# Optimization experiments

Measured on AMD Instinct MI355X. Metric: run time of the kernel, lower is better.

The kernel has to match this reference:

```python
import jax, jax.numpy as jnp
import numpy as np

N_NODES = 100000
N_EDGES = 6400000
D = 12

def setup_inputs() -> dict:
    key = jax.random.key(0)
    k1, k2, k3, k4 = jax.random.split(key, 4)
    x = jax.random.normal(k1, (N_NODES, D), dtype=jnp.float32)
    W_l = jax.random.normal(k2, (D, D), dtype=jnp.float32) / np.sqrt(D)
    W_r = jax.random.normal(k3, (D, D), dtype=jnp.float32) / np.sqrt(D)
    b = jnp.zeros((D,), dtype=jnp.float32)
    edge_index = jax.random.randint(k4, (2, N_EDGES), 0, N_NODES, dtype=jnp.int64)
    return {"x": x, "W_l": W_l, "W_r": W_r, "b": b, "edge_index": edge_index}

def reference(x, W_l, W_r, b, edge_index):
    # PyG SAGEConv (mean aggregation): out = lin_l(mean_{j in N(i)} x_j) + lin_r(x_i)
    src = edge_index[0]
    dst = edge_index[1]
    n = x.shape[0]
    msgs = x[src]                                      # [E, D] gather
    agg = jax.ops.segment_sum(msgs, dst, num_segments=n)          # [N, D]
    cnt = jax.ops.segment_sum(jnp.ones_like(dst, dtype=x.dtype), dst, num_segments=n)
    mean = agg / jnp.maximum(cnt, 1.0)[:, None]        # [N, D]
    out = mean @ W_l.T + x @ W_r.T + b                 # lin_l carries the bias in PyG
    return out
```

## Files before the change

### kernel.cpp

```cpp
#include <hip/hip_runtime.h>

#define N_NODES 100000
#define N_EDGES 6400000
#define D 12

#define SLOG 7
#define SSZ  128
#define NB   ((N_NODES + SSZ - 1) / SSZ)
#define SBLK 256
#define STHR 512
#define SEPB (N_EDGES / SBLK)
#define RSTR 13

#define CAP  1792
#define EPT  (CAP / 256)

__device__ __forceinline__ unsigned int f2bf(float f) {
    unsigned int u = __float_as_uint(f);
    return (u + 0x7fffu + ((u >> 16) & 1u)) >> 16;
}
__device__ __forceinline__ unsigned int pk2(float lo, float hi) {
    return (f2bf(hi) << 16) | f2bf(lo);
}
__device__ __forceinline__ float bflo(unsigned int u) { return __uint_as_float(u << 16); }
__device__ __forceinline__ float bfhi(unsigned int u) { return __uint_as_float(u & 0xffff0000u); }

__global__ __launch_bounds__(256) void prep_kernel(
    const float* __restrict__ x, unsigned int* __restrict__ xb)
{
    int i = blockIdx.x * 256 + threadIdx.x;
    if (i >= N_NODES) return;
    const float4* xr = (const float4*)(x) + (size_t)i * 3;
    float4 a = xr[0], b = xr[1], c = xr[2];
    unsigned int* o = xb + (size_t)i * 8;
    ((uint4*)o)[0] = make_uint4(pk2(a.x, a.y), pk2(a.z, a.w), pk2(b.x, b.y), pk2(b.z, b.w));
    ((uint2*)(o + 4))[0] = make_uint2(pk2(c.x, c.y), pk2(c.z, c.w));
}

__global__ __launch_bounds__(512) void part_kernel(
    const int* __restrict__ ei, int* __restrict__ cnt, int* __restrict__ rowpre,
    unsigned int* __restrict__ sorted)
{
    __shared__ int h[NB];
    __shared__ int cur[NB];
    __shared__ int sb2[512];
    int t = threadIdx.x;
    int b = blockIdx.x;
    for (int i = t; i < NB; i += STHR) h[i] = 0;
    __syncthreads();

    const int* dei = ei + N_EDGES;
    int start = b * SEPB;
    int end = start + SEPB;

    int e = start + t;
    while (e + 3 * STHR < end) {
        int d0 = dei[e], d1 = dei[e + STHR], d2 = dei[e + 2 * STHR], d3 = dei[e + 3 * STHR];
        atomicAdd(&h[d0 >> SLOG], 1);
        atomicAdd(&h[d1 >> SLOG], 1);
        atomicAdd(&h[d2 >> SLOG], 1);
        atomicAdd(&h[d3 >> SLOG], 1);
        e += 4 * STHR;
    }
    while (e < end) { atomicAdd(&h[dei[e] >> SLOG], 1); e += STHR; }
    __syncthreads();

    int* crow = cnt + (size_t)b * NB;
    for (int i = t; i < NB; i += STHR) crow[i] = h[i];

    int pairv = 0;
    if (t < (NB + 1) / 2) {
        pairv = h[2 * t] + ((2 * t + 1 < NB) ? h[2 * t + 1] : 0);
    }
    sb2[t] = pairv;
    __syncthreads();
    for (int o = 1; o < 512; o <<= 1) {
        int v = (t >= o) ? sb2[t - o] : 0;
        __syncthreads();
        sb2[t] += v;
        __syncthreads();
    }
    if (t < (NB + 1) / 2) {
        int excl = sb2[t] - pairv;
        cur[2 * t] = excl;
        if (2 * t + 1 < NB) cur[2 * t + 1] = excl + h[2 * t];
    }
    __syncthreads();

    int* rrow = rowpre + (size_t)b * NB;
    for (int i = t; i < NB; i += STHR) rrow[i] = cur[i];
    __syncthreads();

    unsigned int* dst = sorted + (size_t)b * SEPB;
    e = start + t;
    while (e + 3 * STHR < end) {
        int s0 = ei[e], s1 = ei[e + STHR], s2 = ei[e + 2 * STHR], s3 = ei[e + 3 * STHR];
        int d0 = dei[e], d1 = dei[e + STHR], d2 = dei[e + 2 * STHR], d3 = dei[e + 3 * STHR];
        int p0 = atomicAdd(&cur[d0 >> SLOG], 1);
        int p1 = atomicAdd(&cur[d1 >> SLOG], 1);
        int p2 = atomicAdd(&cur[d2 >> SLOG], 1);
        int p3 = atomicAdd(&cur[d3 >> SLOG], 1);
        dst[p0] = ((unsigned)s0 << SLOG) | (unsigned)(d0 & (SSZ - 1));
        dst[p1] = ((unsigned)s1 << SLOG) | (unsigned)(d1 & (SSZ - 1));
        dst[p2] = ((unsigned)s2 << SLOG) | (unsigned)(d2 & (SSZ - 1));
        dst[p3] = ((unsigned)s3 << SLOG) | (unsigned)(d3 & (SSZ - 1));
        e += 4 * STHR;
    }
    while (e < end) {
        int s = ei[e], d = dei[e];
        int pos = atomicAdd(&cur[d >> SLOG], 1);
        dst[pos] = ((unsigned)s << SLOG) | (unsigned)(d & (SSZ - 1));
        e += STHR;
    }
}

__global__ __launch_bounds__(256) void agg_reg_kernel(
    const unsigned int* __restrict__ sorted, const int* __restrict__ cntm,
    const int* __restrict__ rowpre, const unsigned int* __restrict__ xb,
    const float* __restrict__ x, const float* __restrict__ Wl,
    const float* __restrict__ Wr, const float* __restrict__ bias,
    float* __restrict__ out)
{
    __shared__ float sWl[D * D], sWr[D * D], sb[D];
    __shared__ int cnt[SSZ];
    __shared__ int sbuf[SSZ];
    __shared__ int segbase[SSZ + 1];
    __shared__ int cursor[SSZ];
    __shared__ int cnt_tot[SSZ];
    __shared__ int seglen[SBLK];
    __shared__ int segoff[SBLK];
    __shared__ int segpre[SBLK + 1];
    __shared__ unsigned vals[CAP * 6];

    int t = threadIdx.x;
    int k = blockIdx.x;

    if (t < D * D) { sWl[t] = Wl[t]; sWr[t] = Wr[t]; }
    if (t < D) sb[t] = bias[t];
    if (t < SSZ) cnt_tot[t] = 0;

    if (t < SBLK) {
        seglen[t] = cntm[(size_t)t * NB + k];
        segoff[t] = t * SEPB + rowpre[(size_t)t * NB + k];
    }
    __syncthreads();
    int sl = (t < SBLK) ? seglen[t] : 0;
    if (t < SBLK) sbuf[0] = 0;
    {
        if (t < SBLK) segpre[t + 1] = sl;
        if (t == 0) segpre[0] = 0;
        __syncthreads();
        for (int o = 1; o < SBLK; o <<= 1) {
            int v = 0;
            if (t < SBLK && (int)t + 1 > o) v = segpre[t + 1 - o];
            __syncthreads();
            if (t < SBLK) segpre[t + 1] += v;
            __syncthreads();
        }
    }
    int T = segpre[SBLK];

    float acc[D];
#pragma unroll
    for (int d = 0; d < D; ++d) acc[d] = 0.f;

    int loc = t >> 1;
    int sub = t & 1;

    for (int c0 = 0; c0 < T; c0 += CAP) {
        int n = min(CAP, T - c0);
        if (t < SSZ) cnt[t] = 0;
        __syncthreads();

        unsigned pe[EPT];
        int ne = 0;
        for (int j = t; j < n; j += 256) {
            int v = c0 + j;
            int lo = 0, hi = SBLK;
            while (hi - lo > 1) {
                int mid = (lo + hi) >> 1;
                if (segpre[mid] <= v) lo = mid; else hi = mid;
            }
            int gi = segoff[lo] + (v - segpre[lo]);
            pe[ne++] = sorted[gi];
        }
#pragma unroll
        for (int q = 0; q < EPT; ++q)
            if (q < ne) atomicAdd(&cnt[pe[q] & (SSZ - 1)], 1);
        __syncthreads();

        if (t < SSZ) sbuf[t] = cnt[t];
        __syncthreads();
        for (int o = 1; o < SSZ; o <<= 1) {
            int v = (t < SSZ && t >= o) ? sbuf[t - o] : 0;
            __syncthreads();
            if (t < SSZ) sbuf[t] += v;
            __syncthreads();
        }
        if (t < SSZ) {
            segbase[t + 1] = sbuf[t];
            if (t == 0) segbase[0] = 0;
        }
        __syncthreads();
        if (t < SSZ) { cursor[t] = segbase[t]; cnt_tot[t] += cnt[t]; }
        __syncthreads();

#pragma unroll
        for (int q = 0; q < EPT; ++q) {
            if (q < ne) {
                unsigned p = pe[q];
                int slot = atomicAdd(&cursor[p & (SSZ - 1)], 1);
                const unsigned* r = xb + (size_t)(p >> SLOG) * 8;
                uint2 q0 = ((const uint2*)r)[0];
                uint2 q1 = ((const uint2*)r)[1];
                uint2 q2 = ((const uint2*)r)[2];
                unsigned* vv = &vals[slot * 6];
                ((uint2*)vv)[0] = q0;
                ((uint2*)vv)[1] = q1;
                ((uint2*)vv)[2] = q2;
            }
        }
        __syncthreads();

        int s0 = segbase[loc], s1 = segbase[loc + 1];
        for (int j = s0 + sub; j < s1; j += 2) {
            const unsigned* vv = &vals[j * 6];
            uint2 q0 = ((const uint2*)vv)[0];
            uint2 q1 = ((const uint2*)vv)[1];
            uint2 q2 = ((const uint2*)vv)[2];
            acc[0]  += bflo(q0.x); acc[1]  += bfhi(q0.x);
            acc[2]  += bflo(q0.y); acc[3]  += bfhi(q0.y);
            acc[4]  += bflo(q1.x); acc[5]  += bfhi(q1.x);
            acc[6]  += bflo(q1.y); acc[7]  += bfhi(q1.y);
            acc[8]  += bflo(q2.x); acc[9]  += bfhi(q2.x);
            acc[10] += bflo(q2.y); acc[11] += bfhi(q2.y);
        }
        __syncthreads();
    }

    float* red = (float*)vals;
#pragma unroll
    for (int d = 0; d < D; ++d) red[sub * 1664 + loc * 13 + d] = acc[d];
    __syncthreads();

    if (t < SSZ) {
        int node = k * SSZ + t;
        if (node < N_NODES) {
            float m[D];
#pragma unroll
            for (int d = 0; d < D; ++d)
                m[d] = red[t * 13 + d] + red[1664 + t * 13 + d];
            float inv = 1.f / fmaxf((float)cnt_tot[t], 1.f);
#pragma unroll
            for (int d = 0; d < D; ++d) m[d] *= inv;

            float xi[D];
            const float4* xr = (const float4*)(x) + (size_t)node * 3;
            float4 x0 = xr[0], x1 = xr[1], x2 = xr[2];
            xi[0] = x0.x; xi[1] = x0.y; xi[2]  = x0.z; xi[3]  = x0.w;
            xi[4] = x1.x; xi[5] = x1.y; xi[6]  = x1.z; xi[7]  = x1.w;
            xi[8] = x2.x; xi[9] = x2.y; xi[10] = x2.z; xi[11] = x2.w;

            float o[D];
#pragma unroll
            for (int oo = 0; oo < D; ++oo) {
                float a = sb[oo];
#pragma unroll
                for (int d = 0; d < D; ++d) {
                    a += m[d] * sWl[oo * D + d];
                    a += xi[d] * sWr[oo * D + d];
                }
                o[oo] = a;
            }
            float4* orow = (float4*)(out) + (size_t)node * 3;
            orow[0] = make_float4(o[0], o[1], o[2], o[3]);
            orow[1] = make_float4(o[4], o[5], o[6], o[7]);
            orow[2] = make_float4(o[8], o[9], o[10], o[11]);
        }
    }
}


__global__ __launch_bounds__(256) void scatter_kernel(
    const int* __restrict__ ei, const float* __restrict__ x,
    float* __restrict__ agg, float* __restrict__ cnt)
{
    int e = blockIdx.x * blockDim.x + threadIdx.x;
    if (e >= N_EDGES) return;
    int src = ei[e];
    int dst = ei[N_EDGES + e];
    const float4* xr = (const float4*)(x + (size_t)src * D);
    float4 a = xr[0], b4 = xr[1], c = xr[2];
    float* dr = agg + (size_t)dst * D;
    atomicAdd(dr + 0,  a.x);  atomicAdd(dr + 1,  a.y);
    atomicAdd(dr + 2,  a.z);  atomicAdd(dr + 3,  a.w);
    atomicAdd(dr + 4,  b4.x); atomicAdd(dr + 5,  b4.y);
    atomicAdd(dr + 6,  b4.z); atomicAdd(dr + 7,  b4.w);
    atomicAdd(dr + 8,  c.x);  atomicAdd(dr + 9,  c.y);
    atomicAdd(dr + 10, c.z);  atomicAdd(dr + 11, c.w);
    atomicAdd(cnt + dst, 1.0f);
}

__global__ __launch_bounds__(256) void finalize_kernel(
    const float* __restrict__ x, const float* __restrict__ Wl,
    const float* __restrict__ Wr, const float* __restrict__ bias,
    const float* __restrict__ agg, const float* __restrict__ cnt,
    float* __restrict__ out)
{
    __shared__ float sWl[D * D], sWr[D * D], sb[D];
    int t = threadIdx.x;
    if (t < D * D) { sWl[t] = Wl[t]; sWr[t] = Wr[t]; }
    if (t < D) sb[t] = bias[t];
    __syncthreads();
    int i = blockIdx.x * blockDim.x + t;
    if (i >= N_NODES) return;
    float inv = 1.0f / fmaxf(cnt[i], 1.0f);
    float m[D], xi[D];
    const float4* ar = (const float4*)(agg + (size_t)i * D);
    const float4* xr = (const float4*)(x + (size_t)i * D);
    float4 a0 = ar[0], a1 = ar[1], a2 = ar[2];
    float4 x0 = xr[0], x1 = xr[1], x2 = xr[2];
    m[0] = a0.x * inv; m[1] = a0.y * inv; m[2]  = a0.z * inv; m[3]  = a0.w * inv;
    m[4] = a1.x * inv; m[5] = a1.y * inv; m[6]  = a1.z * inv; m[7]  = a1.w * inv;
    m[8] = a2.x * inv; m[9] = a2.y * inv; m[10] = a2.z * inv; m[11] = a2.w * inv;
    xi[0] = x0.x; xi[1] = x0.y; xi[2]  = x0.z; xi[3]  = x0.w;
    xi[4] = x1.x; xi[5] = x1.y; xi[6]  = x1.z; xi[7]  = x1.w;
    xi[8] = x2.x; xi[9] = x2.y; xi[10] = x2.z; xi[11] = x2.w;
    float o[D];
#pragma unroll
    for (int oo = 0; oo < D; ++oo) {
        float acc = sb[oo];
#pragma unroll
        for (int d = 0; d < D; ++d) {
            acc += m[d] * sWl[oo * D + d];
            acc += xi[d] * sWr[oo * D + d];
        }
        o[oo] = acc;
    }
    float4* orow = (float4*)(out + (size_t)i * D);
    orow[0] = make_float4(o[0], o[1], o[2], o[3]);
    orow[1] = make_float4(o[4], o[5], o[6], o[7]);
    orow[2] = make_float4(o[8], o[9], o[10], o[11]);
}

extern "C" void kernel_launch(void* const* d_in, const int* in_sizes, int n_in,
                              void* d_out, int out_size, void* d_ws, size_t ws_size,
                              hipStream_t stream) {
    const float* x    = (const float*)d_in[0];
    const float* Wl   = (const float*)d_in[1];
    const float* Wr   = (const float*)d_in[2];
    const float* bias = (const float*)d_in[3];
    const int*   ei   = (const int*)d_in[4];
    float* out = (float*)d_out;

    size_t sortedBytes = (size_t)N_EDGES * sizeof(unsigned int);
    size_t xbBytes     = (size_t)N_NODES * 8 * sizeof(unsigned int);
    size_t cntBytes    = (size_t)SBLK * NB * sizeof(int);
    size_t rowpreBytes = cntBytes;
    size_t neededFull = sortedBytes + xbBytes + cntBytes + rowpreBytes;
    size_t neededLast = ((size_t)N_NODES * D + N_NODES) * sizeof(float);

    if (ws_size >= neededFull) {
        char* p = (char*)d_ws;
        unsigned int* sorted = (unsigned int*)p;        p += sortedBytes;
        unsigned int* xb     = (unsigned int*)p;        p += xbBytes;
        int* cnt    = (int*)p;                          p += cntBytes;
        int* rowpre = (int*)p;

        prep_kernel<<<(N_NODES + 255) / 256, 256, 0, stream>>>(x, xb);
        part_kernel<<<SBLK, STHR, 0, stream>>>(ei, cnt, rowpre, sorted);
        agg_reg_kernel<<<NB, 256, 0, stream>>>(sorted, cnt, rowpre, xb, x, Wl, Wr, bias, out);
    } else {
        float* agg = (float*)d_ws;
        float* cnt = agg + (size_t)N_NODES * D;
        hipMemsetAsync(d_ws, 0, neededLast, stream);
        scatter_kernel<<<(N_EDGES + 255) / 256, 256, 0, stream>>>(ei, x, agg, cnt);
        finalize_kernel<<<(N_NODES + 255) / 256, 256, 0, stream>>>(x, Wl, Wr, bias, agg, cnt, out);
    }
}
```

Before: 287.3 us.

## Stage edge indices via coalesced segment copies and pad LDS slots to stride seven

Replaces the per-edge binary search over segment prefixes with a per-wave coalesced copy of contiguous segment ranges into a shared epack buffer, tracked by a sliding segment window. The scatter into LDS now uses an odd stride of 7 words per slot to avoid bank conflicts, and each row is read as one uint4 plus one uint2. CAP shrinks from 1792 to 1280 so the extra LDS buffers fit, which means more chunk iterations and barriers per block. The serial window advance by thread 0 adds a small sequential step per chunk.

```diff
diff --git a/kernel.cpp b/kernel.cpp
--- a/kernel.cpp
+++ b/kernel.cpp
@@ -10,10 +10,9 @@
 #define SBLK 256
 #define STHR 512
 #define SEPB (N_EDGES / SBLK)
-#define RSTR 13
-
-#define CAP  1792
-#define EPT  (CAP / 256)
+
+#define CAP  1280
+#define SLOT 7
 
 __device__ __forceinline__ unsigned int f2bf(float f) {
     unsigned int u = __float_as_uint(f);
@@ -130,7 +129,9 @@
     __shared__ int seglen[SBLK];
     __shared__ int segoff[SBLK];
     __shared__ int segpre[SBLK + 1];
-    __shared__ unsigned vals[CAP * 6];
+    __shared__ int swin;
+    __shared__ unsigned epack[CAP];
+    __shared__ unsigned vals[CAP * SLOT];
 
     int t = threadIdx.x;
     int k = blockIdx.x;
@@ -138,25 +139,22 @@
     if (t < D * D) { sWl[t] = Wl[t]; sWr[t] = Wr[t]; }
     if (t < D) sb[t] = bias[t];
     if (t < SSZ) cnt_tot[t] = 0;
+    if (t == 0) swin = 0;
 
     if (t < SBLK) {
         seglen[t] = cntm[(size_t)t * NB + k];
         segoff[t] = t * SEPB + rowpre[(size_t)t * NB + k];
     }
     __syncthreads();
-    int sl = (t < SBLK) ? seglen[t] : 0;
-    if (t < SBLK) sbuf[0] = 0;
-    {
-        if (t < SBLK) segpre[t + 1] = sl;
-        if (t == 0) segpre[0] = 0;
-        __syncthreads();
-        for (int o = 1; o < SBLK; o <<= 1) {
-            int v = 0;
-            if (t < SBLK && (int)t + 1 > o) v = segpre[t + 1 - o];
-            __syncthreads();
-            if (t < SBLK) segpre[t + 1] += v;
-            __syncthreads();
-        }
+    if (t < SBLK) segpre[t + 1] = seglen[t];
+    if (t == 0) segpre[0] = 0;
+    __syncthreads();
+    for (int o = 1; o < SBLK; o <<= 1) {
+        int v = 0;
+        if (t < SBLK && t + 1 > o) v = segpre[t + 1 - o];
+        __syncthreads();
+        if (t < SBLK) segpre[t + 1] += v;
+        __syncthreads();
     }
     int T = segpre[SBLK];
 
@@ -166,27 +164,37 @@
 
     int loc = t >> 1;
     int sub = t & 1;
+    int wave = t >> 6;
+    int lane = t & 63;
 
     for (int c0 = 0; c0 < T; c0 += CAP) {
         int n = min(CAP, T - c0);
+        int c1 = c0 + n;
+        if (t == 0) {
+            int s = swin;
+            while (segpre[s + 1] <= c0) ++s;
+            swin = s;
+        }
         if (t < SSZ) cnt[t] = 0;
         __syncthreads();
 
-        unsigned pe[EPT];
-        int ne = 0;
-        for (int j = t; j < n; j += 256) {
-            int v = c0 + j;
-            int lo = 0, hi = SBLK;
-            while (hi - lo > 1) {
-                int mid = (lo + hi) >> 1;
-                if (segpre[mid] <= v) lo = mid; else hi = mid;
+        int s0w = swin;
+        for (int s = s0w + wave; s < SBLK && segpre[s] < c1; s += 4) {
+            int vs = segpre[s], ve = segpre[s + 1];
+            int a0 = vs > c0 ? vs : c0;
+            int a1 = ve < c1 ? ve : c1;
+            int len = a1 - a0;
+            if (len > 0) {
+                int goff = segoff[s] + (a0 - vs);
+                int doff = a0 - c0;
+                for (int j = lane; j < len; j += 64)
+                    epack[doff + j] = sorted[goff + j];
             }
-            int gi = segoff[lo] + (v - segpre[lo]);
-            pe[ne++] = sorted[gi];
-        }
-#pragma unroll
-        for (int q = 0; q < EPT; ++q)
-            if (q < ne) atomicAdd(&cnt[pe[q] & (SSZ - 1)], 1);
+        }
+        __syncthreads();
+
+        for (int j = t; j < n; j += 256)
+            atomicAdd(&cnt[epack[j] & (SSZ - 1)], 1);
         __syncthreads();
 
         if (t < SSZ) sbuf[t] = cnt[t];
@@ -205,35 +213,29 @@
         if (t < SSZ) { cursor[t] = segbase[t]; cnt_tot[t] += cnt[t]; }
         __syncthreads();
 
-#pragma unroll
-        for (int q = 0; q < EPT; ++q) {
-            if (q < ne) {
-                unsigned p = pe[q];
-                int slot = atomicAdd(&cursor[p & (SSZ - 1)], 1);
-                const unsigned* r = xb + (size_t)(p >> SLOG) * 8;
-                uint2 q0 = ((const uint2*)r)[0];
-                uint2 q1 = ((const uint2*)r)[1];
-                uint2 q2 = ((const uint2*)r)[2];
-                unsigned* vv = &vals[slot * 6];
-                ((uint2*)vv)[0] = q0;
-                ((uint2*)vv)[1] = q1;
-                ((uint2*)vv)[2] = q2;
-            }
+        for (int j = t; j < n; j += 256) {
+            unsigned p = epack[j];
+            int slot = atomicAdd(&cursor[p & (SSZ - 1)], 1);
+            const unsigned* r = xb + (size_t)(p >> SLOG) * 8;
+            uint4 q01 = ((const uint4*)r)[0];
+            uint2 w2  = ((const uint2*)(r + 4))[0];
+            unsigned* vv = &vals[slot * SLOT];
+            vv[0] = q01.x; vv[1] = q01.y; vv[2] = q01.z;
+            vv[3] = q01.w; vv[4] = w2.x;  vv[5] = w2.y;
         }
         __syncthreads();
 
         int s0 = segbase[loc], s1 = segbase[loc + 1];
         for (int j = s0 + sub; j < s1; j += 2) {
-            const unsigned* vv = &vals[j * 6];
-            uint2 q0 = ((const uint2*)vv)[0];
-            uint2 q1 = ((const uint2*)vv)[1];
-            uint2 q2 = ((const uint2*)vv)[2];
-            acc[0]  += bflo(q0.x); acc[1]  += bfhi(q0.x);
-            acc[2]  += bflo(q0.y); acc[3]  += bfhi(q0.y);
-            acc[4]  += bflo(q1.x); acc[5]  += bfhi(q1.x);
-            acc[6]  += bflo(q1.y); acc[7]  += bfhi(q1.y);
-            acc[8]  += bflo(q2.x); acc[9]  += bfhi(q2.x);
-            acc[10] += bflo(q2.y); acc[11] += bfhi(q2.y);
+            const unsigned* vv = &vals[j * SLOT];
+            unsigned a0 = vv[0], a1 = vv[1], a2 = vv[2];
+            unsigned a3 = vv[3], a4 = vv[4], a5 = vv[5];
+            acc[0]  += bflo(a0); acc[1]  += bfhi(a0);
+            acc[2]  += bflo(a1); acc[3]  += bfhi(a1);
+            acc[4]  += bflo(a2); acc[5]  += bfhi(a2);
+            acc[6]  += bflo(a3); acc[7]  += bfhi(a3);
+            acc[8]  += bflo(a4); acc[9]  += bfhi(a4);
+            acc[10] += bflo(a5); acc[11] += bfhi(a5);
         }
         __syncthreads();
     }
```

Result: slower. 325.9 us (+13.4%).
